# Kernel optimization log

Measured on AMD Instinct MI355X. Metric: run time of the kernel, lower is better.

Reference implementation:

```python
import jax, jax.numpy as jnp
import numpy as np

BN_EPS = 1e-5


def setup_inputs() -> dict:
    key = jax.random.key(0)
    ks = jax.random.split(key, 9)
    B, C, H, W = 2, 64, 128, 128
    Ci = 32  # inter_channels
    sc = 0.05
    x = jax.random.normal(ks[0], (B, C, H, W), jnp.float32)
    g_w = jax.random.normal(ks[1], (Ci, C), jnp.float32) * sc
    g_b = jax.random.normal(ks[2], (Ci,), jnp.float32) * sc
    theta_w = jax.random.normal(ks[3], (Ci, C), jnp.float32) * sc
    theta_b = jax.random.normal(ks[4], (Ci,), jnp.float32) * sc
    phi_w = jax.random.normal(ks[5], (Ci, C), jnp.float32) * sc
    phi_b = jax.random.normal(ks[6], (Ci,), jnp.float32) * sc
    w_w = jax.random.normal(ks[7], (C, Ci), jnp.float32) * sc
    w_b = jnp.zeros((C,), jnp.float32)
    # BatchNorm affine params (random so the block is non-trivial; the torch
    # code zero-inits them, which would make the whole block an identity).
    bn_gamma = 1.0 + 0.1 * jax.random.normal(ks[8], (C,), jnp.float32)
    bn_beta = jnp.zeros((C,), jnp.float32)
    return dict(x=x, g_w=g_w, g_b=g_b, theta_w=theta_w, theta_b=theta_b,
                phi_w=phi_w, phi_b=phi_b, w_w=w_w, w_b=w_b,
                bn_gamma=bn_gamma, bn_beta=bn_beta)


def reference(x, g_w, g_b, theta_w, theta_b, phi_w, phi_b, w_w, w_b,
              bn_gamma, bn_beta):
    B, C, H, W = x.shape
    Ci = g_w.shape[0]
    H1, W1 = H // 2, W // 2

    def block(xq):  # embedded-gaussian non-local block on one quadrant group [B,C,h,w]
        b, c, h, w = xq.shape
        n = h * w
        xf = xq.reshape(b, c, n)                                  # [B,C,N]
        th = jnp.einsum('oc,bcn->bno', theta_w, xf) + theta_b     # [B,N,Ci]
        ph = jnp.einsum('oc,bcn->bon', phi_w, xf) + phi_b[:, None]  # [B,Ci,N]
        gx = jnp.einsum('oc,bcn->bno', g_w, xf) + g_b             # [B,N,Ci]
        f = jnp.einsum('bno,bom->bnm', th, ph)                    # [B,N,N] affinity
        a = jax.nn.softmax(f, axis=-1)
        y = jnp.einsum('bnm,bmo->bno', a, gx)                     # [B,N,Ci]
        wy = jnp.einsum('co,bno->bcn', w_w, y) + w_b[:, None]     # [B,C,N]
        wy = wy.reshape(b, c, h, w)
        # BatchNorm2d, training-mode batch stats (per quadrant call in torch)
        mu = wy.mean(axis=(0, 2, 3), keepdims=True)
        var = wy.var(axis=(0, 2, 3), keepdims=True)
        bn = (wy - mu) * jax.lax.rsqrt(var + BN_EPS)
        bn = bn * bn_gamma[None, :, None, None] + bn_beta[None, :, None, None]
        return bn + xq                                            # residual

    # split into 4 quadrants: [B,C,H,W] -> [4,B,C,H1,W1] (quadrant-major)
    xq = x.reshape(B, C, 2, H1, 2, W1).transpose(2, 4, 0, 1, 3, 5)
    xq = xq.reshape(4, B, C, H1, W1)
    zq = jax.vmap(block)(xq)                                      # [4,B,C,H1,W1]
    # reassemble
    z = zq.reshape(2, 2, B, C, H1, W1).transpose(2, 3, 0, 4, 1, 5)
    return z.reshape(B, C, H, W)
```

## Files before the change

### kernel.cpp

```cpp
#include <hip/hip_runtime.h>
#include <stdint.h>

typedef __bf16 bf16x8 __attribute__((ext_vector_type(8)));
typedef short  short4v __attribute__((ext_vector_type(4)));
typedef float  floatx4 __attribute__((ext_vector_type(4)));
typedef uint32_t u32x4 __attribute__((ext_vector_type(4)));

#define DI __device__ __forceinline__

DI uint16_t f2bf(float f) {
    union { float f; uint32_t i; } v; v.f = f;
    uint32_t u = v.i;
    return (uint16_t)((u + 0x7FFFu + ((u >> 16) & 1u)) >> 16);
}
DI uint32_t packbf2(float a, float b) {
    return __builtin_amdgcn_perm(__float_as_uint(b) + 0x8000u,
                                 __float_as_uint(a) + 0x8000u, 0x07060302u);
}

__global__ __launch_bounds__(256) void proj_kernel(
    const float* __restrict__ x,
    const float* __restrict__ tw, const float* __restrict__ tb,
    const float* __restrict__ pw, const float* __restrict__ pb,
    const float* __restrict__ gw, const float* __restrict__ gb,
    uint16_t* __restrict__ th, uint16_t* __restrict__ phT,
    uint16_t* __restrict__ vP)
{
    __shared__ uint16_t ldsg[32 * 68];
    int nt = blockIdx.x & 63, blk = blockIdx.x >> 6;
    int tid = threadIdx.x, wid = tid >> 6, lane = tid & 63;
    int quad = lane >> 4, low = lane & 15;

    int b = blk & 1, q = blk >> 1, qh = q >> 1, qw = q & 1;
    int pixA = wid * 16 + low;
    const float* xg = x + (size_t)b * 1048576 +
                      (size_t)(qh * 64 + nt) * 128 + qw * 64 + pixA;

    float a0[8], a1[8];
#pragma unroll
    for (int j = 0; j < 8; ++j) {
        a0[j] = xg[(size_t)(quad * 8 + j) * 16384];
        a1[j] = xg[(size_t)(32 + quad * 8 + j) * 16384];
    }
    union { uint32_t u[4]; bf16x8 v; } A0, A1;
#pragma unroll
    for (int j = 0; j < 4; ++j) {
        A0.u[j] = packbf2(a0[2*j], a0[2*j+1]);
        A1.u[j] = packbf2(a1[2*j], a1[2*j+1]);
    }

    auto dotile = [&](const float* W, const float* Bv, int o0) -> floatx4 {
        floatx4 acc;
        float bias = Bv[o0 + low];
#pragma unroll
        for (int r = 0; r < 4; ++r) acc[r] = bias;
        const float* wr = W + (o0 + low) * 64 + quad * 8;
        floatx4 w0a = *(const floatx4*)(wr);
        floatx4 w0b = *(const floatx4*)(wr + 4);
        floatx4 w1a = *(const floatx4*)(wr + 32);
        floatx4 w1b = *(const floatx4*)(wr + 36);
        union { uint32_t u[4]; bf16x8 v; } B0, B1;
        B0.u[0] = packbf2(w0a[0], w0a[1]); B0.u[1] = packbf2(w0a[2], w0a[3]);
        B0.u[2] = packbf2(w0b[0], w0b[1]); B0.u[3] = packbf2(w0b[2], w0b[3]);
        B1.u[0] = packbf2(w1a[0], w1a[1]); B1.u[1] = packbf2(w1a[2], w1a[3]);
        B1.u[2] = packbf2(w1b[0], w1b[1]); B1.u[3] = packbf2(w1b[2], w1b[3]);
        acc = __builtin_amdgcn_mfma_f32_16x16x32_bf16(A0.v, B0.v, acc, 0, 0, 0);
        acc = __builtin_amdgcn_mfma_f32_16x16x32_bf16(A1.v, B1.v, acc, 0, 0, 0);
        return acc;
    };

    size_t thbase = ((size_t)blk * 4096 + nt * 64 + wid * 16 + quad * 4) * 32;

    floatx4 t0 = dotile(tw, tb, 0), t1 = dotile(tw, tb, 16);
#pragma unroll
    for (int r = 0; r < 4; ++r) {
        th[thbase + r * 32 + low]      = f2bf(t0[r] * 1.44269504088896f);
        th[thbase + r * 32 + 16 + low] = f2bf(t1[r] * 1.44269504088896f);
    }
    floatx4 p0 = dotile(pw, pb, 0), p1 = dotile(pw, pb, 16);
#pragma unroll
    for (int r = 0; r < 4; ++r) {
        phT[thbase + r * 32 + low]      = f2bf(p0[r]);
        phT[thbase + r * 32 + 16 + low] = f2bf(p1[r]);
    }
    floatx4 g0 = dotile(gw, gb, 0), g1 = dotile(gw, gb, 16);
#pragma unroll
    for (int r = 0; r < 4; ++r) {
        ldsg[(low)      * 68 + wid * 16 + quad * 4 + r] = f2bf(g0[r]);
        ldsg[(16 + low) * 68 + wid * 16 + quad * 4 + r] = f2bf(g1[r]);
    }
    __syncthreads();
    {
        int o = tid >> 3, k = (tid & 7) * 8;
        const uint16_t* src = &ldsg[o * 68 + k];
        uint64_t lo = *(const uint64_t*)(src);
        uint64_t hi = *(const uint64_t*)(src + 4);
        union { uint64_t q[2]; u32x4 v; } out;
        out.q[0] = lo; out.q[1] = hi;
        *(u32x4*)(vP + (size_t)blk * 131072 + nt * 2048 + tid * 8) = out.v;
    }
}

__global__ __launch_bounds__(256, 2) void flash_kernel(
    const uint16_t* __restrict__ th, const uint16_t* __restrict__ phT,
    const uint16_t* __restrict__ vP, const float* __restrict__ w_w,
    const float* __restrict__ w_b, float* __restrict__ wy,
    float2* __restrict__ partials)
{
    __shared__ uint16_t ldsK[2][2][64 * 40];
    __shared__ uint16_t ldsV[2][2][32 * 72];
    __shared__ float sred[4][64][2];
    int rg  = blockIdx.x & 63;
    int blk = blockIdx.x >> 6;
    int tid = threadIdx.x, wid = tid >> 6, lane = tid & 63;
    int quad = lane >> 4, low = lane & 15;
    int n0 = rg * 64 + wid * 16;

    const uint16_t* thB = th  + (size_t)blk * 131072;
    const uint16_t* kG  = phT + (size_t)blk * 131072;
    const uint16_t* vG  = vP  + (size_t)blk * 131072;

    bf16x8 qf = *(const bf16x8*)(thB + (n0 + low) * 32 + quad * 8);

    const int kWr = (tid >> 2) * 40 + (tid & 3) * 8;
    const int vWr = (tid >> 3) * 72 + (tid & 7) * 8;
    const u32x4* kSrc = (const u32x4*)kG + tid;
    const u32x4* vSrc = (const u32x4*)vG + tid;

    u32x4 kr0 = kSrc[0],  kr1 = kSrc[256];
    u32x4 vr0 = vSrc[0],  vr1 = vSrc[256];
    *(u32x4*)(&ldsK[0][0][kWr]) = kr0;  *(u32x4*)(&ldsK[0][1][kWr]) = kr1;
    *(u32x4*)(&ldsV[0][0][vWr]) = vr0;  *(u32x4*)(&ldsV[0][1][vWr]) = vr1;
    __syncthreads();

    floatx4 zero = {0.f, 0.f, 0.f, 0.f};
    floatx4 oa0 = zero, oa1 = zero, os = zero;
    union { uint32_t u[2]; short4v v; } ones;
    ones.u[0] = 0x3F803F80u; ones.u[1] = 0x3F803F80u;

    for (int t = 0; t < 32; ++t) {
        int buf = t & 1;
        if (t < 31) {
            kr0 = kSrc[(2*t + 2) * 256]; kr1 = kSrc[(2*t + 3) * 256];
            vr0 = vSrc[(2*t + 2) * 256]; vr1 = vSrc[(2*t + 3) * 256];
        }
#pragma unroll
        for (int s = 0; s < 2; ++s) {
            const uint16_t* Kb = ldsK[buf][s];
            const uint16_t* Vb = ldsV[buf][s];
            bf16x8  kf[4]; short4v va[4], vb[4];
#pragma unroll
            for (int c = 0; c < 4; ++c) {
                kf[c] = *(const bf16x8*)(Kb + (c * 16 + low) * 40 + quad * 8);
                va[c] = *(const short4v*)(Vb + low * 72 + c * 16 + quad * 4);
                vb[c] = *(const short4v*)(Vb + (16 + low) * 72 + c * 16 + quad * 4);
            }
            floatx4 sa[4];
#pragma unroll
            for (int c = 0; c < 4; ++c)
                sa[c] = __builtin_amdgcn_mfma_f32_16x16x32_bf16(kf[c], qf, zero, 0, 0, 0);
            union { uint32_t u[2]; short4v v; } P[4];
#pragma unroll
            for (int c = 0; c < 4; ++c) {
                float p0 = __builtin_amdgcn_exp2f(sa[c][0]);
                float p1 = __builtin_amdgcn_exp2f(sa[c][1]);
                float p2 = __builtin_amdgcn_exp2f(sa[c][2]);
                float p3 = __builtin_amdgcn_exp2f(sa[c][3]);
                P[c].u[0] = packbf2(p0, p1);
                P[c].u[1] = packbf2(p2, p3);
            }
#pragma unroll
            for (int c = 0; c < 4; ++c) {
                oa0 = __builtin_amdgcn_mfma_f32_16x16x16bf16_1k(va[c], P[c].v, oa0, 0, 0, 0);
                oa1 = __builtin_amdgcn_mfma_f32_16x16x16bf16_1k(vb[c], P[c].v, oa1, 0, 0, 0);
                os  = __builtin_amdgcn_mfma_f32_16x16x16bf16_1k(ones.v, P[c].v, os, 0, 0, 0);
            }
        }
        if (t < 31) {
            *(u32x4*)(&ldsK[buf ^ 1][0][kWr]) = kr0;
            *(u32x4*)(&ldsK[buf ^ 1][1][kWr]) = kr1;
            *(u32x4*)(&ldsV[buf ^ 1][0][vWr]) = vr0;
            *(u32x4*)(&ldsV[buf ^ 1][1][vWr]) = vr1;
        }
        __syncthreads();
    }

    float rinv = 1.0f / os[0];
    union { uint32_t u[2]; short4v v; } Y0, Y1;
    Y0.u[0] = packbf2(oa0[0] * rinv, oa0[1] * rinv);
    Y0.u[1] = packbf2(oa0[2] * rinv, oa0[3] * rinv);
    Y1.u[0] = packbf2(oa1[0] * rinv, oa1[1] * rinv);
    Y1.u[1] = packbf2(oa1[2] * rinv, oa1[3] * rinv);

    float* wyB = wy + (size_t)blk * 262144;
    int n = n0 + low;
#pragma unroll
    for (int ct = 0; ct < 4; ++ct) {
        floatx4 acc;
#pragma unroll
        for (int r = 0; r < 4; ++r) acc[r] = w_b[ct * 16 + quad * 4 + r];
        floatx4 w0 = *(const floatx4*)(w_w + (ct * 16 + low) * 32 + quad * 4);
        floatx4 w1 = *(const floatx4*)(w_w + (ct * 16 + low) * 32 + 16 + quad * 4);
        union { uint32_t u[2]; short4v v; } W0, W1;
        W0.u[0] = packbf2(w0[0], w0[1]); W0.u[1] = packbf2(w0[2], w0[3]);
        W1.u[0] = packbf2(w1[0], w1[1]); W1.u[1] = packbf2(w1[2], w1[3]);
        acc = __builtin_amdgcn_mfma_f32_16x16x16bf16_1k(W0.v, Y0.v, acc, 0, 0, 0);
        acc = __builtin_amdgcn_mfma_f32_16x16x16bf16_1k(W1.v, Y1.v, acc, 0, 0, 0);
#pragma unroll
        for (int r = 0; r < 4; ++r) {
            wyB[(size_t)(ct * 16 + quad * 4 + r) * 4096 + n] = acc[r];
            float s = acc[r], ss = acc[r] * acc[r];
            s += __shfl_xor(s, 1); ss += __shfl_xor(ss, 1);
            s += __shfl_xor(s, 2); ss += __shfl_xor(ss, 2);
            s += __shfl_xor(s, 4); ss += __shfl_xor(ss, 4);
            s += __shfl_xor(s, 8); ss += __shfl_xor(ss, 8);
            if (low == 0) {
                sred[wid][ct * 16 + quad * 4 + r][0] = s;
                sred[wid][ct * 16 + quad * 4 + r][1] = ss;
            }
        }
    }
    __syncthreads();
    if (tid < 64) {
        float s  = sred[0][tid][0] + sred[1][tid][0] + sred[2][tid][0] + sred[3][tid][0];
        float ss = sred[0][tid][1] + sred[1][tid][1] + sred[2][tid][1] + sred[3][tid][1];
        partials[(size_t)blockIdx.x * 64 + tid] = make_float2(s, ss);
    }
}

__global__ __launch_bounds__(256) void stats_kernel(
    const float2* __restrict__ partials, const float* __restrict__ gamma,
    const float* __restrict__ beta, float2* __restrict__ stats)
{
    int q = blockIdx.x;
    int c = threadIdx.x & 63, g = threadIdx.x >> 6;
    float S = 0.f, SS = 0.f;
    for (int w = g; w < 128; w += 4) {
        int wg = (q * 2 + (w >> 6)) * 64 + (w & 63);
        float2 p = partials[(size_t)wg * 64 + c];
        S += p.x; SS += p.y;
    }
    __shared__ float sh[2][4][64];
    sh[0][g][c] = S; sh[1][g][c] = SS;
    __syncthreads();
    if (threadIdx.x < 64) {
        int cc = threadIdx.x;
        float St  = sh[0][0][cc] + sh[0][1][cc] + sh[0][2][cc] + sh[0][3][cc];
        float SSt = sh[1][0][cc] + sh[1][1][cc] + sh[1][2][cc] + sh[1][3][cc];
        float mu  = St * (1.0f / 8192.0f);
        float var = SSt * (1.0f / 8192.0f) - mu * mu;
        float scale = gamma[cc] * rsqrtf(var + 1e-5f);
        float shift = beta[cc] - mu * scale;
        stats[q * 64 + cc] = make_float2(scale, shift);
    }
}

__global__ __launch_bounds__(256) void final_kernel(
    const float* __restrict__ wy, const float2* __restrict__ stats,
    const float* __restrict__ x, float* __restrict__ out)
{
    size_t base = ((size_t)blockIdx.x * 256 + threadIdx.x) * 4;
    int n   = (int)(base & 4095);
    int c   = (int)((base >> 12) & 63);
    int blk = (int)(base >> 18);
    int b = blk & 1, q = blk >> 1, qh = q >> 1, qw = q & 1;
    int i = n >> 6, j = n & 63;
    float2 sc = stats[q * 64 + c];
    floatx4 wv = *(const floatx4*)(wy + base);
    size_t xa = ((size_t)(b * 64 + c) * 128 + (qh * 64 + i)) * 128 + qw * 64 + j;
    floatx4 xv = *(const floatx4*)(x + xa);
    floatx4 ov;
#pragma unroll
    for (int k = 0; k < 4; ++k) ov[k] = wv[k] * sc.x + sc.y + xv[k];
    *(floatx4*)(out + xa) = ov;
}

extern "C" void kernel_launch(void* const* d_in, const int* in_sizes, int n_in,
                              void* d_out, int out_size, void* d_ws, size_t ws_size,
                              hipStream_t stream)
{
    const float* x       = (const float*)d_in[0];
    const float* g_w     = (const float*)d_in[1];
    const float* g_b     = (const float*)d_in[2];
    const float* theta_w = (const float*)d_in[3];
    const float* theta_b = (const float*)d_in[4];
    const float* phi_w   = (const float*)d_in[5];
    const float* phi_b   = (const float*)d_in[6];
    const float* w_w     = (const float*)d_in[7];
    const float* w_b     = (const float*)d_in[8];
    const float* gamma   = (const float*)d_in[9];
    const float* beta    = (const float*)d_in[10];

    char* ws = (char*)d_ws;
    uint16_t* th       = (uint16_t*)(ws);
    uint16_t* phT      = (uint16_t*)(ws + (2u << 20));
    uint16_t* vP       = (uint16_t*)(ws + (4u << 20));
    float*    wy       = (float*)(ws + (6u << 20));
    float2*   partials = (float2*)(ws + (14u << 20));
    float2*   stats    = (float2*)(ws + (14u << 20) + (1u << 18));

    proj_kernel  <<<512,  256, 0, stream>>>(x, theta_w, theta_b, phi_w, phi_b,
                                            g_w, g_b, th, phT, vP);
    flash_kernel <<<512,  256, 0, stream>>>(th, phT, vP, w_w, w_b, wy, partials);
    stats_kernel <<<4,    256, 0, stream>>>(partials, gamma, beta, stats);
    final_kernel <<<2048, 256, 0, stream>>>(wy, stats, x, (float*)d_out);
}
```

Baseline: 138.8 us.

## Split key range across two wave groups per block and merge partial accumulators

The flash kernel now runs 512 threads per block, and the two halves each process half of the key/value sequence, with separate LDS double buffers per half. After the loop the halves exchange their unnormalized output and row-sum accumulators through LDS, and each half then computes two of the four output channel tiles. The block index mapping changes so that batch-quadrant varies fastest. This is meant to halve the serial loop length per wave and raise the number of resident waves, at the cost of more LDS per block, one extra exchange barrier, and no max-subtraction in the merge (the exp2 values are simply summed).

```diff
diff --git a/kernel.cpp b/kernel.cpp
--- a/kernel.cpp
+++ b/kernel.cpp
@@ -101,20 +101,22 @@
     }
 }
 
-__global__ __launch_bounds__(256, 2) void flash_kernel(
+__global__ __launch_bounds__(512, 4) void flash_kernel(
     const uint16_t* __restrict__ th, const uint16_t* __restrict__ phT,
     const uint16_t* __restrict__ vP, const float* __restrict__ w_w,
     const float* __restrict__ w_b, float* __restrict__ wy,
     float2* __restrict__ partials)
 {
-    __shared__ uint16_t ldsK[2][2][64 * 40];
-    __shared__ uint16_t ldsV[2][2][32 * 72];
+    __shared__ uint16_t ldsK[2][2][2][64 * 40];
+    __shared__ uint16_t ldsV[2][2][2][32 * 72];
     __shared__ float sred[4][64][2];
-    int rg  = blockIdx.x & 63;
-    int blk = blockIdx.x >> 6;
+    int blk = blockIdx.x & 7;
+    int rg  = blockIdx.x >> 3;
     int tid = threadIdx.x, wid = tid >> 6, lane = tid & 63;
+    int half = wid >> 2, w4 = wid & 3;
+    int ltid = tid & 255;
     int quad = lane >> 4, low = lane & 15;
-    int n0 = rg * 64 + wid * 16;
+    int n0 = rg * 64 + w4 * 16;
 
     const uint16_t* thB = th  + (size_t)blk * 131072;
     const uint16_t* kG  = phT + (size_t)blk * 131072;
@@ -122,15 +124,15 @@
 
     bf16x8 qf = *(const bf16x8*)(thB + (n0 + low) * 32 + quad * 8);
 
-    const int kWr = (tid >> 2) * 40 + (tid & 3) * 8;
-    const int vWr = (tid >> 3) * 72 + (tid & 7) * 8;
-    const u32x4* kSrc = (const u32x4*)kG + tid;
-    const u32x4* vSrc = (const u32x4*)vG + tid;
+    const int kWr = (ltid >> 2) * 40 + (ltid & 3) * 8;
+    const int vWr = (ltid >> 3) * 72 + (ltid & 7) * 8;
+    const u32x4* kSrc = (const u32x4*)kG + half * 8192 + ltid;
+    const u32x4* vSrc = (const u32x4*)vG + half * 8192 + ltid;
 
     u32x4 kr0 = kSrc[0],  kr1 = kSrc[256];
     u32x4 vr0 = vSrc[0],  vr1 = vSrc[256];
-    *(u32x4*)(&ldsK[0][0][kWr]) = kr0;  *(u32x4*)(&ldsK[0][1][kWr]) = kr1;
-    *(u32x4*)(&ldsV[0][0][vWr]) = vr0;  *(u32x4*)(&ldsV[0][1][vWr]) = vr1;
+    *(u32x4*)(&ldsK[half][0][0][kWr]) = kr0;  *(u32x4*)(&ldsK[half][0][1][kWr]) = kr1;
+    *(u32x4*)(&ldsV[half][0][0][vWr]) = vr0;  *(u32x4*)(&ldsV[half][0][1][vWr]) = vr1;
     __syncthreads();
 
     floatx4 zero = {0.f, 0.f, 0.f, 0.f};
@@ -138,16 +140,16 @@
     union { uint32_t u[2]; short4v v; } ones;
     ones.u[0] = 0x3F803F80u; ones.u[1] = 0x3F803F80u;
 
-    for (int t = 0; t < 32; ++t) {
+    for (int t = 0; t < 16; ++t) {
         int buf = t & 1;
-        if (t < 31) {
+        if (t < 15) {
             kr0 = kSrc[(2*t + 2) * 256]; kr1 = kSrc[(2*t + 3) * 256];
             vr0 = vSrc[(2*t + 2) * 256]; vr1 = vSrc[(2*t + 3) * 256];
         }
 #pragma unroll
         for (int s = 0; s < 2; ++s) {
-            const uint16_t* Kb = ldsK[buf][s];
-            const uint16_t* Vb = ldsV[buf][s];
+            const uint16_t* Kb = ldsK[half][buf][s];
+            const uint16_t* Vb = ldsV[half][buf][s];
             bf16x8  kf[4]; short4v va[4], vb[4];
 #pragma unroll
             for (int c = 0; c < 4; ++c) {
@@ -176,16 +178,35 @@
                 os  = __builtin_amdgcn_mfma_f32_16x16x16bf16_1k(ones.v, P[c].v, os, 0, 0, 0);
             }
         }
-        if (t < 31) {
-            *(u32x4*)(&ldsK[buf ^ 1][0][kWr]) = kr0;
-            *(u32x4*)(&ldsK[buf ^ 1][1][kWr]) = kr1;
-            *(u32x4*)(&ldsV[buf ^ 1][0][vWr]) = vr0;
-            *(u32x4*)(&ldsV[buf ^ 1][1][vWr]) = vr1;
+        if (t < 15) {
+            *(u32x4*)(&ldsK[half][buf ^ 1][0][kWr]) = kr0;
+            *(u32x4*)(&ldsK[half][buf ^ 1][1][kWr]) = kr1;
+            *(u32x4*)(&ldsV[half][buf ^ 1][0][vWr]) = vr0;
+            *(u32x4*)(&ldsV[half][buf ^ 1][1][vWr]) = vr1;
         }
         __syncthreads();
     }
 
-    float rinv = 1.0f / os[0];
+    {
+        float* exM = (float*)(&ldsK[half][0][0][0]);
+        int li9 = ltid * 9;
+#pragma unroll
+        for (int r = 0; r < 4; ++r) {
+            exM[li9 + r]     = oa0[r];
+            exM[li9 + 4 + r] = oa1[r];
+        }
+        exM[li9 + 8] = os[0];
+    }
+    __syncthreads();
+    const float* exO = (const float*)(&ldsK[half ^ 1][0][0][0]);
+    float os0 = os[0] + exO[ltid * 9 + 8];
+#pragma unroll
+    for (int r = 0; r < 4; ++r) {
+        oa0[r] += exO[ltid * 9 + r];
+        oa1[r] += exO[ltid * 9 + 4 + r];
+    }
+
+    float rinv = 1.0f / os0;
     union { uint32_t u[2]; short4v v; } Y0, Y1;
     Y0.u[0] = packbf2(oa0[0] * rinv, oa0[1] * rinv);
     Y0.u[1] = packbf2(oa0[2] * rinv, oa0[3] * rinv);
@@ -195,7 +216,8 @@
     float* wyB = wy + (size_t)blk * 262144;
     int n = n0 + low;
 #pragma unroll
-    for (int ct = 0; ct < 4; ++ct) {
+    for (int cc = 0; cc < 2; ++cc) {
+        int ct = half * 2 + cc;
         floatx4 acc;
 #pragma unroll
         for (int r = 0; r < 4; ++r) acc[r] = w_b[ct * 16 + quad * 4 + r];
@@ -215,8 +237,8 @@
             s += __shfl_xor(s, 4); ss += __shfl_xor(ss, 4);
             s += __shfl_xor(s, 8); ss += __shfl_xor(ss, 8);
             if (low == 0) {
-                sred[wid][ct * 16 + quad * 4 + r][0] = s;
-                sred[wid][ct * 16 + quad * 4 + r][1] = ss;
+                sred[w4][ct * 16 + quad * 4 + r][0] = s;
+                sred[w4][ct * 16 + quad * 4 + r][1] = ss;
             }
         }
     }
@@ -224,7 +246,7 @@
     if (tid < 64) {
         float s  = sred[0][tid][0] + sred[1][tid][0] + sred[2][tid][0] + sred[3][tid][0];
         float ss = sred[0][tid][1] + sred[1][tid][1] + sred[2][tid][1] + sred[3][tid][1];
-        partials[(size_t)blockIdx.x * 64 + tid] = make_float2(s, ss);
+        partials[((size_t)blk * 64 + rg) * 64 + tid] = make_float2(s, ss);
     }
 }
 
@@ -301,7 +323,7 @@
 
     proj_kernel  <<<512,  256, 0, stream>>>(x, theta_w, theta_b, phi_w, phi_b,
                                             g_w, g_b, th, phT, vP);
-    flash_kernel <<<512,  256, 0, stream>>>(th, phT, vP, w_w, w_b, wy, partials);
+    flash_kernel <<<512,  512, 0, stream>>>(th, phT, vP, w_w, w_b, wy, partials);
     stats_kernel <<<4,    256, 0, stream>>>(partials, gamma, beta, stats);
     final_kernel <<<2048, 256, 0, stream>>>(wy, stats, x, (float*)d_out);
 }
```

Measured after the change: 138.2 us. No clear change (-0.5%).
